# Optimization experiments

Measured on AMD Instinct MI355X. Metric: run time of the kernel, lower is better.

## Reference

```python
import jax, jax.numpy as jnp
import numpy as np

N_H = 896
N_EMB = 300
V_IN = 30000
V_OUT = 30000
B = 64
T_ENC = 40
T_DEC = 40


def gru_cell(x, h, Wih, Whh, bih, bhh):
    # PyTorch GRU cell math
    gi = x @ Wih.T + bih          # [B, 3H]
    gh = h @ Whh.T + bhh          # [B, 3H]
    ir, iz, inn = jnp.split(gi, 3, axis=-1)
    hr, hz, hn = jnp.split(gh, 3, axis=-1)
    r = jax.nn.sigmoid(ir + hr)
    z = jax.nn.sigmoid(iz + hz)
    n = jnp.tanh(inn + r * hn)
    return (1.0 - z) * n + z * h


def run_gru(xs, h0, Wih, Whh, bih, bhh, reverse=False):
    # xs: [T, B, E] -> outputs [T, B, H], final hidden [B, H]
    def step(h, x):
        h2 = gru_cell(x, h, Wih, Whh, bih, bhh)
        return h2, h2
    hT, ys = jax.lax.scan(step, h0, xs, reverse=reverse)
    return ys, hT


def setup_inputs() -> dict:
    key = jax.random.key(0)
    ks = jax.random.split(key, 20)
    s = 0.05
    inp = {
        'x_encoder': jax.random.randint(ks[0], (B, T_ENC), 0, V_IN - 1),
        'x_decoder': jax.random.randint(ks[1], (B, T_DEC), 0, V_OUT - 1),
        'emb_enc': jax.random.normal(ks[2], (V_IN, N_EMB), jnp.float32) * s,
        'Wih_f': jax.random.normal(ks[3], (3 * N_H, N_EMB), jnp.float32) * s,
        'Whh_f': jax.random.normal(ks[4], (3 * N_H, N_H), jnp.float32) * s,
        'bih_f': jnp.zeros((3 * N_H,), jnp.float32),
        'bhh_f': jnp.zeros((3 * N_H,), jnp.float32),
        'Wih_b': jax.random.normal(ks[5], (3 * N_H, N_EMB), jnp.float32) * s,
        'Whh_b': jax.random.normal(ks[6], (3 * N_H, N_H), jnp.float32) * s,
        'bih_b': jnp.zeros((3 * N_H,), jnp.float32),
        'bhh_b': jnp.zeros((3 * N_H,), jnp.float32),
        'emb_dec': jax.random.normal(ks[7], (V_OUT, N_EMB), jnp.float32) * s,
        'Wih_d': jax.random.normal(ks[8], (3 * N_H, N_EMB), jnp.float32) * s,
        'Whh_d': jax.random.normal(ks[9], (3 * N_H, N_H), jnp.float32) * s,
        'bih_d': jnp.zeros((3 * N_H,), jnp.float32),
        'bhh_d': jnp.zeros((3 * N_H,), jnp.float32),
        'fc_W': jax.random.normal(ks[10], (V_OUT, 2 * N_H), jnp.float32) * s,
        'fc_b': jnp.zeros((V_OUT,), jnp.float32),
    }
    return inp


def reference(x_encoder, x_decoder, emb_enc, Wih_f, Whh_f, bih_f, bhh_f,
              Wih_b, Whh_b, bih_b, bhh_b, emb_dec, Wih_d, Whh_d, bih_d,
              bhh_d, fc_W, fc_b):
    Bsz = x_encoder.shape[0]
    h0 = jnp.zeros((Bsz, N_H), jnp.float32)

    # ---- Encoder: bidirectional 1-layer GRU (no padding, full lengths) ----
    xs = emb_enc[x_encoder].transpose(1, 0, 2)          # [Te, B, E]
    y_f, h_f = run_gru(xs, h0, Wih_f, Whh_f, bih_f, bhh_f)
    y_b, h_b = run_gru(xs, h0, Wih_b, Whh_b, bih_b, bhh_b, reverse=True)
    y_enc = (y_f + y_b).transpose(1, 0, 2)              # [B, Te, H] (dirs summed)
    h = h_f + h_b                                       # [B, H]

    # ---- Decoder: per-step GRU + dot-product attention over encoder ----
    xd = emb_dec[x_decoder].transpose(1, 0, 2)          # [Td, B, E]

    def dec_step(h, x):
        h2 = gru_cell(x, h, Wih_d, Whh_d, bih_d, bhh_d)        # [B, H]
        scores = jnp.einsum('bth,bh->bt', y_enc, h2)           # ed_mat
        attn = jax.nn.softmax(scores, axis=1)                  # over Te
        ctx = jnp.einsum('bt,bth->bh', attn, y_enc)            # [B, H]
        logits = jnp.concatenate([h2, ctx], axis=-1) @ fc_W.T + fc_b
        return h2, jax.nn.softmax(logits, axis=-1)

    _, ys = jax.lax.scan(dec_step, h, xd)               # [Td, B, V]
    return ys.transpose(1, 0, 2)                        # [B, Td, V]
```

## Files before the change

### kernel.cpp

```cpp
#include <hip/hip_runtime.h>

#define BB 64
#define TE 40
#define TD 40
#define ED 300
#define EP 320
#define HD 896
#define G3 2688
#define VO 30000
#define VP2 30208
#define KZ 1792
#define KT 28
#define MR 2560
#define NBLK 120

#define FOFF 0
#define BOFF 56
#define DOFF 112
#define AOFF 168
#define TOFF 232
#define FSTR 32

typedef __attribute__((ext_vector_type(8))) __bf16 bf16x8;
typedef __attribute__((ext_vector_type(4))) float f32x4;
typedef __attribute__((ext_vector_type(4))) unsigned int u32x4;
typedef __attribute__((ext_vector_type(4))) unsigned short u16x4;

typedef __attribute__((address_space(1))) const void av1c;
typedef __attribute__((address_space(3))) void av3;

__device__ __forceinline__ float sig_(float x)  { return 1.0f / (1.0f + __expf(-x)); }
__device__ __forceinline__ float tanh_(float x) { return 1.0f - 2.0f / (__expf(2.0f * x) + 1.0f); }

__device__ __forceinline__ void gload_lds16(const __bf16* g, __bf16* l) {
    __builtin_amdgcn_global_load_lds((av1c*)g, (av3*)l, 16, 0, 0);
}

__device__ __forceinline__ bf16x8 ld128_sc(const __bf16* p) {
    bf16x8 r;
    asm volatile("global_load_dwordx4 %0, %1, off sc0 sc1" : "=v"(r) : "v"(p));
    return r;
}
__device__ __forceinline__ f32x4 ldf4_sc(const float* p) {
    f32x4 r;
    asm volatile("global_load_dwordx4 %0, %1, off sc0 sc1" : "=v"(r) : "v"(p));
    return r;
}
__device__ __forceinline__ float ldf_sc(const float* p) {
    float r;
    asm volatile("global_load_dword %0, %1, off sc0 sc1" : "=v"(r) : "v"(p));
    return r;
}
__device__ __forceinline__ void vm_wait0() {
    asm volatile("s_waitcnt vmcnt(0)" ::: "memory");
}
__device__ __forceinline__ void stf_sc(float* p, float v) {
    asm volatile("global_store_dword %0, %1, off sc0 sc1" :: "v"(p), "v"(v) : "memory");
}
__device__ __forceinline__ void sth_sc(__bf16* p, float v) {
    unsigned int u = (unsigned int)__builtin_bit_cast(unsigned short, (__bf16)v);
    asm volatile("global_store_short %0, %1, off sc0 sc1" :: "v"(p), "v"(u) : "memory");
}
__device__ __forceinline__ void sti_sc(int* p, int v) {
    asm volatile("global_store_dword %0, %1, off sc0 sc1" :: "v"(p), "v"(v) : "memory");
}
__device__ __forceinline__ void spin_ge(const int* p, int target) {
    int v;
    for (;;) {
        asm volatile("global_load_dword %0, %1, off sc0 sc1\n\ts_waitcnt vmcnt(0)"
                     : "=v"(v) : "v"(p) : "memory");
        if (v >= target) break;
        __builtin_amdgcn_s_sleep(1);
    }
}

__device__ __forceinline__ size_t hblk(int b, int c) {
    return ((size_t)(c >> 4) * 64 + b) * 16 + (c & 15);
}

__device__ __forceinline__ void stage_w(__bf16* wlds, const float* __restrict__ W, int c0)
{
    const int tid = threadIdx.x;
    for (int ch = tid; ch < 48 * 224; ch += 256) {
        const int lr = ch / 224, c4 = (ch % 224) * 4;
        const int g = lr >> 4, rr = lr & 15;
        const int kk = c4 >> 5, hi = (c4 & 31) >> 3, j = c4 & 7;
        const float4 v = *(const float4*)&W[(size_t)(g * HD + c0 + rr) * HD + c4];
        __bf16* d = &wlds[((g * 28 + kk) * 64 + hi * 16 + rr) * 8 + j];
        d[0] = (__bf16)v.x; d[1] = (__bf16)v.y; d[2] = (__bf16)v.z; d[3] = (__bf16)v.w;
    }
}

struct GiReg { float g0[4], g1[4], g2[4]; };

__device__ __forceinline__ GiReg gi_prefetch(const float* __restrict__ GIt,
                                             int c, int w, int hi)
{
    GiReg r;
#pragma unroll
    for (int rg = 0; rg < 4; ++rg) {
        const float* gp = GIt + (size_t)(16 * w + hi * 4 + rg) * G3 + c;
        r.g0[rg] = gp[0]; r.g1[rg] = gp[HD]; r.g2[rg] = gp[2 * HD];
    }
    return r;
}

__device__ __forceinline__ void gru_step(
    const __bf16* __restrict__ hcurB, const float* __restrict__ hcurF,
    const __bf16* __restrict__ wlds, const GiReg& gi,
    float bh0, float bh1, float bh2,
    float* __restrict__ hnF, __bf16* __restrict__ hnB,
    float* __restrict__ yencD,
    int tt,
    __bf16* __restrict__ zrow,
    int c0, int lane, int w)
{
    const int r16 = lane & 15, hi = lane >> 4;
    const int c = c0 + r16;
    const int colblk = c0 >> 4;
    const int brow = 16 * w;

    bf16x8 afr[28];
    const __bf16* ap = hcurB + ((size_t)(hi >> 1) * 64 + brow + r16) * 16 + (hi & 1) * 8;
#pragma unroll
    for (int kk = 0; kk < 28; ++kk) afr[kk] = ld128_sc(ap + kk * 2048);
    float hp[4];
#pragma unroll
    for (int rg = 0; rg < 4; ++rg)
        hp[rg] = ldf_sc(hcurF + ((size_t)colblk * 64 + brow + hi * 4 + rg) * 16 + r16);
    vm_wait0();
    __builtin_amdgcn_sched_barrier(0);

    f32x4 a0 = {0.f, 0.f, 0.f, 0.f}, a1 = a0, a2 = a0;
#pragma unroll
    for (int kk = 0; kk < 28; ++kk) {
        const bf16x8 b0 = *(const bf16x8*)&wlds[(kk) * 512 + lane * 8];
        const bf16x8 b1 = *(const bf16x8*)&wlds[(28 + kk) * 512 + lane * 8];
        const bf16x8 b2 = *(const bf16x8*)&wlds[(56 + kk) * 512 + lane * 8];
        a0 = __builtin_amdgcn_mfma_f32_16x16x32_bf16(afr[kk], b0, a0, 0, 0, 0);
        a1 = __builtin_amdgcn_mfma_f32_16x16x32_bf16(afr[kk], b1, a1, 0, 0, 0);
        a2 = __builtin_amdgcn_mfma_f32_16x16x32_bf16(afr[kk], b2, a2, 0, 0, 0);
    }

#pragma unroll
    for (int rg = 0; rg < 4; ++rg) {
        const int b = brow + hi * 4 + rg;
        const float rr = sig_(gi.g0[rg] + a0[rg] + bh0);
        const float zz = sig_(gi.g1[rg] + a1[rg] + bh1);
        const float nn = tanh_(gi.g2[rg] + rr * (a2[rg] + bh2));
        const float hnew = (1.0f - zz) * nn + zz * hp[rg];
        const size_t so = ((size_t)colblk * 64 + b) * 16 + r16;
        stf_sc(hnF + so, hnew);
        sth_sc(hnB + so, hnew);
        if (yencD) stf_sc(yencD + (((size_t)colblk * 64 + b) * TE + tt) * 16 + r16, hnew);
        if (zrow)  zrow[(size_t)b * KZ + c] = (__bf16)hnew;
    }
}

__device__ __forceinline__ void attn_step(
    const float* __restrict__ yencL, float* __restrict__ h2s,
    float* __restrict__ scL, float* __restrict__ attwL,
    const float* __restrict__ h2g, int b, __bf16* __restrict__ zr,
    int* __restrict__ myflag, int postval)
{
    const int tid = threadIdx.x, lane = tid & 63, w = tid >> 6;

    const float a0 = ldf_sc(h2g + hblk(b, tid));
    const float a1 = ldf_sc(h2g + hblk(b, tid + 256));
    const float a2 = ldf_sc(h2g + hblk(b, tid + 512));
    const float a3 = (tid < HD - 768) ? ldf_sc(h2g + hblk(b, tid + 768)) : 0.0f;
    vm_wait0();
    __builtin_amdgcn_sched_barrier(0);
    h2s[tid] = a0; h2s[tid + 256] = a1; h2s[tid + 512] = a2;
    if (tid < HD - 768) h2s[tid + 768] = a3;
    __syncthreads();
    if (tid == 0) sti_sc(myflag, postval);

    const float2* h22 = (const float2*)h2s;
    for (int t = w; t < TE; t += 4) {
        const float2* y2 = (const float2*)(yencL + t * HD);
        float p = 0.f;
#pragma unroll
        for (int it = 0; it < HD / 128; ++it) {
            const float2 ya = y2[lane + it * 64];
            const float2 hb2 = h22[lane + it * 64];
            p += ya.x * hb2.x + ya.y * hb2.y;
        }
        p += __shfl_down(p, 32); p += __shfl_down(p, 16); p += __shfl_down(p, 8);
        p += __shfl_down(p, 4);  p += __shfl_down(p, 2);  p += __shfl_down(p, 1);
        if (lane == 0) scL[t] = p;
    }
    __syncthreads();

    float m = scL[0];
    for (int t = 1; t < TE; ++t) m = fmaxf(m, scL[t]);
    float s = 0.f;
    for (int t = 0; t < TE; ++t) s += __expf(scL[t] - m);
    const float inv = 1.0f / s;
    if (tid < TE) attwL[tid] = __expf(scL[tid] - m) * inv;
    __syncthreads();

    for (int c = tid; c < HD; c += 256) {
        float acc = 0.f;
#pragma unroll
        for (int t = 0; t < TE; ++t) acc += attwL[t] * yencL[t * HD + c];
        zr[(size_t)b * KZ + HD + c] = (__bf16)acc;
    }
    __syncthreads();
}

__global__ __launch_bounds__(256, 1) void recur(
    const float* __restrict__ GIf, const float* __restrict__ GIb,
    const float* __restrict__ GId,
    const float* __restrict__ WhhF, const float* __restrict__ WhhB,
    const float* __restrict__ WhhD,
    const float* __restrict__ bhhF, const float* __restrict__ bhhB,
    const float* __restrict__ bhhD,
    float* __restrict__ heF, __bf16* __restrict__ heB,
    float* __restrict__ hdF, __bf16* __restrict__ hdB,
    float* __restrict__ yenc_f, float* __restrict__ yenc_b,
    __bf16* __restrict__ Zb, int* __restrict__ flags)
{
    __shared__ __align__(16) char smem[147456];
    __bf16* wlds  = (__bf16*)smem;
    float*  yencL = (float*)smem;
    float*  h2s   = (float*)(smem + 143360);
    float*  scL   = (float*)(smem + 146944);
    float*  attwL = (float*)(smem + 147136);

    const int gid = blockIdx.x;
    const int tid = threadIdx.x;
    const int lane = tid & 63, w = tid >> 6;
    const int r16 = lane & 15, hi = lane >> 4;
    const size_t S = (size_t)BB * HD;

    float bb0 = 0.f, bb1 = 0.f, bb2 = 0.f;
    GiReg gi;

    if (gid < 112) {
        const int dir = (gid >= 56) ? 1 : 0;
        const int gloc = dir ? gid - 56 : gid;
        const int c0e = gloc * 16;
        const float* GIe  = dir ? GIb : GIf;
        const float* bhhE = dir ? bhhB : bhhF;
        float* yencD = dir ? yenc_b : yenc_f;
        const int foff = dir ? BOFF : FOFF;

        stage_w(wlds, dir ? WhhB : WhhF, c0e);
        const int ce = c0e + r16;
        bb0 = bhhE[ce]; bb1 = bhhE[HD + ce]; bb2 = bhhE[2 * HD + ce];
        gi = gi_prefetch(GIe + (size_t)(dir ? TE - 1 : 0) * BB * G3, ce, w, hi);
        __syncthreads();

        for (int t = 0; t < TE; ++t) {
            if (t > 0) {
                if (tid < 56) spin_ge(flags + (foff + tid) * FSTR, t);
                __syncthreads();
            }
            GiReg gin = gi;
            if (t + 1 < TE) {
                const int ttn = dir ? (TE - 2 - t) : (t + 1);
                gin = gi_prefetch(GIe + (size_t)ttn * BB * G3, ce, w, hi);
            }
            const int tt = dir ? (TE - 1 - t) : t;
            gru_step(heB + (size_t)(dir * 2 + (t & 1)) * S,
                     heF + (size_t)(dir * 2 + (t & 1)) * S,
                     wlds, gi, bb0, bb1, bb2,
                     heF + (size_t)(dir * 2 + ((t + 1) & 1)) * S,
                     heB + (size_t)(dir * 2 + ((t + 1) & 1)) * S,
                     yencD, tt, nullptr, c0e, lane, w);
            vm_wait0();
            __syncthreads();
            if (tid == 0) sti_sc(flags + (foff + gloc) * FSTR, t + 1);
            gi = gin;
        }
    }

    if (tid < 112) spin_ge(flags + tid * FSTR, TE);
    __syncthreads();

    {
        const int i0 = gid * 256 + tid;
        const int i1 = i0 + NBLK * 256;
        const bool has1 = (i1 < BB * HD);
        const float f0 = ldf_sc(&heF[0 * S + i0]);
        const float b0 = ldf_sc(&heF[2 * S + i0]);
        const float f1 = has1 ? ldf_sc(&heF[0 * S + i1]) : 0.f;
        const float b1 = has1 ? ldf_sc(&heF[2 * S + i1]) : 0.f;
        vm_wait0();
        __builtin_amdgcn_sched_barrier(0);
        const float v0 = f0 + b0;
        stf_sc(&hdF[i0], v0); sth_sc(&hdB[i0], v0);
        if (has1) { const float v1 = f1 + b1; stf_sc(&hdF[i1], v1); sth_sc(&hdB[i1], v1); }
    }
    if (gid < 56) {
        stage_w(wlds, WhhD, gid * 16);
        const int cd = gid * 16 + r16;
        bb0 = bhhD[cd]; bb1 = bhhD[HD + cd]; bb2 = bhhD[2 * HD + cd];
        gi = gi_prefetch(GId, cd, w, hi);
    }
    vm_wait0();
    __syncthreads();
    if (tid == 0) sti_sc(flags + (TOFF + gid) * FSTR, 1);
    if (tid < 120) spin_ge(flags + (TOFF + tid) * FSTR, 1);
    __syncthreads();

    if (gid < 56) {
        for (int p = 0; p < TD; ++p) {
            if (p > 0 && tid < 56) spin_ge(flags + (DOFF + tid) * FSTR, p);
            if (p >= 4 && tid >= 64 && tid < 128)
                spin_ge(flags + (AOFF + tid - 64) * FSTR, p - 3);
            __syncthreads();
            GiReg gin = gi;
            if (p + 1 < TD)
                gin = gi_prefetch(GId + (size_t)(p + 1) * BB * G3, gid * 16 + r16, w, hi);
            gru_step(hdB + (size_t)(p & 3) * S, hdF + (size_t)(p & 3) * S,
                     wlds, gi, bb0, bb1, bb2,
                     hdF + (size_t)((p + 1) & 3) * S, hdB + (size_t)((p + 1) & 3) * S,
                     nullptr, 0, Zb + (size_t)p * BB * KZ, gid * 16, lane, w);
            vm_wait0();
            __syncthreads();
            if (tid == 0) sti_sc(flags + (DOFF + gid) * FSTR, p + 1);
            gi = gin;
        }
    } else {
        const int b = gid - 56;
        const float* sf = yenc_f;
        const float* sb = yenc_b;
        for (int it = 0; it < 7; ++it) {
            const int i = it * 1280 + tid;
            f32x4 a_[5], b_[5];
            int g_[5], t_[5], c_[5];
#pragma unroll
            for (int u = 0; u < 5; ++u) {
                const int j = i + u * 256;
                g_[u] = j / 160;
                const int rem = j - g_[u] * 160;
                t_[u] = rem >> 2;
                c_[u] = (rem & 3) * 4;
                const size_t sa = (((size_t)g_[u] * 64 + b) * TE + t_[u]) * 16 + c_[u];
                a_[u] = ldf4_sc(sf + sa);
                b_[u] = ldf4_sc(sb + sa);
            }
            vm_wait0();
            __builtin_amdgcn_sched_barrier(0);
#pragma unroll
            for (int u = 0; u < 5; ++u)
                *(f32x4*)&yencL[(size_t)t_[u] * HD + g_[u] * 16 + c_[u]] = a_[u] + b_[u];
        }
        __syncthreads();
        for (int s = 0; s < TD; ++s) {
            if (tid < 56) spin_ge(flags + (DOFF + tid) * FSTR, s + 1);
            __syncthreads();
            attn_step(yencL, h2s, scL, attwL, hdF + (size_t)((s + 1) & 3) * S,
                      b, Zb + (size_t)s * BB * KZ, flags + (AOFF + b) * FSTR, s + 1);
        }
    }
}

__global__ __launch_bounds__(256) void gemm_bt(
    const __bf16* __restrict__ A0, const __bf16* __restrict__ B0,
    float* __restrict__ C0, const float* __restrict__ bias0,
    const __bf16* __restrict__ A1, const __bf16* __restrict__ B1,
    float* __restrict__ C1, const float* __restrict__ bias1,
    int M, int N, int K)
{
    constexpr int BM = 128, BN = 128, BK = 32;
    constexpr int FM = 4, FN = 4;

    const __bf16* A = A0; const __bf16* Bp = B0;
    float* C = C0; const float* bias = bias0;
    if (blockIdx.z == 1) { A = A1; Bp = B1; C = C1; bias = bias1; }

    __shared__ __bf16 Ash[2][BM * BK];
    __shared__ __bf16 Bsh[2][BN * BK];

    const int tid  = threadIdx.x;
    const int lane = tid & 63;
    const int wave = tid >> 6;
    const int wr = wave >> 1, wc = wave & 1;

    const int nwg = gridDim.x * gridDim.y;
    const int orig = blockIdx.y * gridDim.x + blockIdx.x;
    const int q = nwg >> 3, r = nwg & 7;
    const int xcd = orig & 7, idx = orig >> 3;
    const int wg = (xcd < r ? xcd * (q + 1) : r * (q + 1) + (xcd - r) * q) + idx;
    const int mtiles = gridDim.y;
    const long tileM = (long)(wg % mtiles) * BM;
    const long tileN = (long)(wg / mtiles) * BN;

    const int r16 = lane & 15;
    const int hi  = lane >> 4;

    f32x4 acc[FM][FN];
    const f32x4 zero = {0.f, 0.f, 0.f, 0.f};
#pragma unroll
    for (int m = 0; m < FM; ++m)
#pragma unroll
        for (int n = 0; n < FN; ++n) acc[m][n] = zero;

    const int srow = wave * 32 + (lane >> 2);
    const int schunk = (lane & 3) * 8;
    const __bf16* gA = A + (size_t)(tileM + srow) * K + schunk;
    const __bf16* gB = Bp + (size_t)(tileN + srow) * K + schunk;
    const size_t kstep16 = (size_t)16 * K;
    const int lofs = (wave * 32) * BK;

#define STAGE_T(k0_, sel_)                                            \
    do {                                                              \
        gload_lds16(gA + (k0_), &Ash[sel_][lofs]);                    \
        gload_lds16(gA + (k0_) + kstep16, &Ash[sel_][lofs + 16 * BK]);\
        gload_lds16(gB + (k0_), &Bsh[sel_][lofs]);                    \
        gload_lds16(gB + (k0_) + kstep16, &Bsh[sel_][lofs + 16 * BK]);\
    } while (0)

    STAGE_T(0, 0);
    int cur = 0;
    for (int k0 = BK; k0 < K; k0 += BK) {
        STAGE_T(k0, cur ^ 1);
        asm volatile("s_waitcnt vmcnt(4)" ::: "memory");
        __builtin_amdgcn_s_barrier();
        __builtin_amdgcn_sched_barrier(0);

        bf16x8 af[FM], bfr[FN];
#pragma unroll
        for (int m = 0; m < FM; ++m)
            af[m] = *(const bf16x8*)&Ash[cur][(wr * 64 + m * 16 + r16) * BK + hi * 8];
#pragma unroll
        for (int n = 0; n < FN; ++n)
            bfr[n] = *(const bf16x8*)&Bsh[cur][(wc * 64 + n * 16 + r16) * BK + hi * 8];
#pragma unroll
        for (int m = 0; m < FM; ++m)
#pragma unroll
            for (int n = 0; n < FN; ++n)
                acc[m][n] = __builtin_amdgcn_mfma_f32_16x16x32_bf16(af[m], bfr[n], acc[m][n], 0, 0, 0);

        __builtin_amdgcn_sched_barrier(0);
        __builtin_amdgcn_s_barrier();
        __builtin_amdgcn_sched_barrier(0);
        cur ^= 1;
    }
    asm volatile("s_waitcnt vmcnt(0)" ::: "memory");
    __builtin_amdgcn_s_barrier();
    __builtin_amdgcn_sched_barrier(0);
    {
        bf16x8 af[FM], bfr[FN];
#pragma unroll
        for (int m = 0; m < FM; ++m)
            af[m] = *(const bf16x8*)&Ash[cur][(wr * 64 + m * 16 + r16) * BK + hi * 8];
#pragma unroll
        for (int n = 0; n < FN; ++n)
            bfr[n] = *(const bf16x8*)&Bsh[cur][(wc * 64 + n * 16 + r16) * BK + hi * 8];
#pragma unroll
        for (int m = 0; m < FM; ++m)
#pragma unroll
            for (int n = 0; n < FN; ++n)
                acc[m][n] = __builtin_amdgcn_mfma_f32_16x16x32_bf16(af[m], bfr[n], acc[m][n], 0, 0, 0);
    }
#undef STAGE_T

#pragma unroll
    for (int m = 0; m < FM; ++m) {
#pragma unroll
        for (int n = 0; n < FN; ++n) {
            const long gcol = tileN + wc * 64 + n * 16 + r16;
            const float bv = bias ? bias[gcol] : 0.0f;
#pragma unroll
            for (int rr = 0; rr < 4; ++rr) {
                const long grow = tileM + wr * 64 + m * 16 + hi * 4 + rr;
                C[grow * N + gcol] = acc[m][n][rr] + bv;
            }
        }
    }
}

__global__ __launch_bounds__(512, 2) void gemm_fc(
    const __bf16* __restrict__ A,
    const __bf16* __restrict__ B,
    float* __restrict__ C,
    const float* __restrict__ bias)
{
    __shared__ __bf16 lds[65536];

    const int tid = threadIdx.x;
    const int lane = tid & 63;
    const int wave = tid >> 6;
    const int wm = wave >> 2;
    const int wn = wave & 3;
    const int r16 = lane & 15, hi = lane >> 4;

    const int nwg = gridDim.x * gridDim.y;
    const int orig = blockIdx.y * gridDim.x + blockIdx.x;
    const int q_ = nwg >> 3, r_ = nwg & 7;
    const int xcd = orig & 7, idx = orig >> 3;
    const int wg = (xcd < r_ ? xcd * (q_ + 1) : r_ * (q_ + 1) + (xcd - r_) * q_) + idx;
    const int mtiles = gridDim.y;
    const long tileM = (long)(wg % mtiles) * 256;
    const long tileN = (long)(wg / mtiles) * 256;

    const int srow0 = wave * 8 + (lane >> 3);
    const int scol  = ((lane & 7) ^ (lane >> 3)) * 8;
    const __bf16* gAh[2] = { A + (size_t)tileM * KZ, A + (size_t)(tileM + 128) * KZ };
    const __bf16* gBh[2] = { B + (size_t)tileN * KZ, B + (size_t)(tileN + 128) * KZ };
    auto Abase = [](int buf, int h) { return (buf * 2 + h) * 8192; };
    auto Bbase = [](int buf, int h) { return 32768 + (buf * 2 + h) * 8192; };
    auto stage = [&](const __bf16* gph, int kt, int lbase) {
        const __bf16* g0 = gph + (size_t)srow0 * KZ + kt * 64 + scol;
        gload_lds16(g0, &lds[lbase + wave * 512]);
        gload_lds16(g0 + (size_t)64 * KZ, &lds[lbase + (8 + wave) * 512]);
    };
    const int cbx0 = (((0 * 64) + hi * 16) ^ ((r16 & 7) << 4)) >> 1;
    const int cbx1 = (((1 * 64) + hi * 16) ^ ((r16 & 7) << 4)) >> 1;

    f32x4 acc[8][4];
    const f32x4 zero = {0.f, 0.f, 0.f, 0.f};
#pragma unroll
    for (int m = 0; m < 8; ++m)
#pragma unroll
        for (int n = 0; n < 4; ++n) acc[m][n] = zero;

    stage(gAh[0], 0, Abase(0, 0));
    stage(gAh[1], 0, Abase(0, 1));
    stage(gBh[0], 0, Bbase(0, 0));
    stage(gBh[1], 0, Bbase(0, 1));
    stage(gBh[0], 1, Bbase(1, 0));
    stage(gBh[1], 1, Bbase(1, 1));
    asm volatile("s_waitcnt vmcnt(4)" ::: "memory");
    __builtin_amdgcn_s_barrier();

    for (int kt = 0; kt < KT; ++kt) {
        const int buf = kt & 1;
        const int kn1 = (kt + 1 < KT) ? kt + 1 : 0;
        const int kn2 = (kt + 2 < KT) ? kt + 2 : 0;
        const int Ab = Abase(buf, wm);
        const int Bb = Bbase(buf, wn >> 1);
        bf16x8 bfr[4][2];
#pragma unroll
        for (int q = 0; q < 4; ++q) {
            if (q == 0) {
#pragma unroll
                for (int n = 0; n < 4; ++n) {
                    const int rowB = (wn & 1) * 64 + n * 16 + r16;
                    bfr[n][0] = *(const bf16x8*)&lds[Bb + rowB * 64 + cbx0];
                    bfr[n][1] = *(const bf16x8*)&lds[Bb + rowB * 64 + cbx1];
                }
            }
            bf16x8 af[2][2];
#pragma unroll
            for (int mm = 0; mm < 2; ++mm) {
                const int rowA = (q * 2 + mm) * 16 + r16;
                af[mm][0] = *(const bf16x8*)&lds[Ab + rowA * 64 + cbx0];
                af[mm][1] = *(const bf16x8*)&lds[Ab + rowA * 64 + cbx1];
            }
            if (q == 0)      stage(gAh[0], kn1, Abase(buf ^ 1, 0));
            else if (q == 1) stage(gAh[1], kn1, Abase(buf ^ 1, 1));
            else if (q == 2) stage(gBh[0], kn2, Bbase(buf, 0));
            else {
                stage(gBh[1], kn2, Bbase(buf, 1));
                asm volatile("s_waitcnt vmcnt(4)" ::: "memory");
            }
            __builtin_amdgcn_s_barrier();
            asm volatile("s_waitcnt lgkmcnt(0)" ::: "memory");
            __builtin_amdgcn_sched_barrier(0);
            __builtin_amdgcn_s_setprio(1);
#pragma unroll
            for (int mm = 0; mm < 2; ++mm)
#pragma unroll
                for (int n = 0; n < 4; ++n) {
                    acc[q * 2 + mm][n] = __builtin_amdgcn_mfma_f32_16x16x32_bf16(
                        af[mm][0], bfr[n][0], acc[q * 2 + mm][n], 0, 0, 0);
                    acc[q * 2 + mm][n] = __builtin_amdgcn_mfma_f32_16x16x32_bf16(
                        af[mm][1], bfr[n][1], acc[q * 2 + mm][n], 0, 0, 0);
                }
            __builtin_amdgcn_s_setprio(0);
            __builtin_amdgcn_sched_barrier(0);
            __builtin_amdgcn_s_barrier();
        }
    }
    asm volatile("s_waitcnt vmcnt(0)" ::: "memory");

#pragma unroll
    for (int m = 0; m < 8; ++m) {
#pragma unroll
        for (int n = 0; n < 4; ++n) {
            const long gcol = tileN + wn * 64 + n * 16 + r16;
            if (gcol >= VO) continue;
            const float bv = bias[gcol];
#pragma unroll
            for (int rr = 0; rr < 4; ++rr) {
                const long grow = tileM + wm * 128 + m * 16 + hi * 4 + rr;
                const long t = grow >> 6, b = grow & 63;
                C[(b * TD + t) * VO + gcol] = acc[m][n][rr] + bv;
            }
        }
    }
}

__global__ __launch_bounds__(256) void conv_pad(const float* __restrict__ src,
                                                __bf16* __restrict__ dst,
                                                int Rout, int Rin, int Kout, int Kin)
{
    size_t i = (size_t)blockIdx.x * 256 + threadIdx.x;
    const size_t total = (size_t)Rout * Kout;
    const size_t stride = (size_t)gridDim.x * 256;
    for (; i < total; i += stride) {
        int k = (int)(i % Kout);
        int r = (int)(i / Kout);
        float v = (r < Rin && k < Kin) ? src[(size_t)r * Kin + k] : 0.0f;
        dst[i] = (__bf16)v;
    }
}

__global__ __launch_bounds__(256) void conv_fcw(const float* __restrict__ src,
                                                __bf16* __restrict__ dst)
{
    const size_t total4 = (size_t)VP2 * KZ / 4;
    for (size_t i = (size_t)blockIdx.x * 256 + threadIdx.x; i < total4;
         i += (size_t)gridDim.x * 256) {
        const size_t e0 = i * 4;
        const int r = (int)(e0 / KZ);
        u16x4 o;
        if (r < VO) {
            const float4 x = *(const float4*)&src[e0];
            o.x = __builtin_bit_cast(unsigned short, (__bf16)x.x);
            o.y = __builtin_bit_cast(unsigned short, (__bf16)x.y);
            o.z = __builtin_bit_cast(unsigned short, (__bf16)x.z);
            o.w = __builtin_bit_cast(unsigned short, (__bf16)x.w);
        } else {
            o.x = 0; o.y = 0; o.z = 0; o.w = 0;
        }
        *(u16x4*)&dst[e0] = o;
    }
}

__global__ __launch_bounds__(256) void gather_embed(const int* __restrict__ tok,
                                                    const float* __restrict__ emb,
                                                    __bf16* __restrict__ X)
{
    int i = blockIdx.x * 256 + threadIdx.x;
    const int total = TE * BB * EP;
    for (; i < total; i += gridDim.x * 256) {
        int e = i % EP;
        int row = i / EP;
        int t = row >> 6, b = row & 63;
        float v = 0.0f;
        if (e < ED) v = emb[(size_t)tok[b * TE + t] * ED + e];
        X[i] = (__bf16)v;
    }
}

__global__ __launch_bounds__(1024) void softmax_kernel(float* __restrict__ out)
{
    __shared__ float row[VO];
    __shared__ float red[16];
    __shared__ float red2[16];
    const size_t base = (size_t)blockIdx.x * VO;
    const int tid = threadIdx.x;
    const int lane = tid & 63, w = tid >> 6;

    float m = -1e30f;
    for (int ch = tid; ch < VO / 4; ch += 1024) {
        const float4 x = *(const float4*)&out[base + ch * 4];
        *(float4*)&row[ch * 4] = x;
        m = fmaxf(fmaxf(fmaxf(m, x.x), x.y), fmaxf(x.z, x.w));
    }
    m = fmaxf(m, __shfl_down(m, 32)); m = fmaxf(m, __shfl_down(m, 16));
    m = fmaxf(m, __shfl_down(m, 8));  m = fmaxf(m, __shfl_down(m, 4));
    m = fmaxf(m, __shfl_down(m, 2));  m = fmaxf(m, __shfl_down(m, 1));
    if (lane == 0) red[w] = m;
    __syncthreads();
    if (tid == 0) {
        float mm = red[0];
#pragma unroll
        for (int i = 1; i < 16; ++i) mm = fmaxf(mm, red[i]);
        red[0] = mm;
    }
    __syncthreads();
    m = red[0];

    float s = 0.0f;
    for (int v = tid; v < VO; v += 1024) {
        const float e = __expf(row[v] - m);
        row[v] = e;
        s += e;
    }
    s += __shfl_down(s, 32); s += __shfl_down(s, 16); s += __shfl_down(s, 8);
    s += __shfl_down(s, 4);  s += __shfl_down(s, 2);  s += __shfl_down(s, 1);
    if (lane == 0) red2[w] = s;
    __syncthreads();
    if (tid == 0) {
        float ss = red2[0];
#pragma unroll
        for (int i = 1; i < 16; ++i) ss += red2[i];
        red2[0] = ss;
    }
    __syncthreads();
    s = red2[0];

    const float inv = 1.0f / s;
    for (int ch = tid; ch < VO / 4; ch += 1024) {
        float4 x = *(const float4*)&row[ch * 4];
        x.x *= inv; x.y *= inv; x.z *= inv; x.w *= inv;
        *(float4*)&out[base + ch * 4] = x;
    }
}

extern "C" void kernel_launch(void* const* d_in, const int* in_sizes, int n_in,
                              void* d_out, int out_size, void* d_ws, size_t ws_size,
                              hipStream_t stream)
{
    if (n_in < 18) return;
    const int*   x_enc   = (const int*)d_in[0];
    const int*   x_dec   = (const int*)d_in[1];
    const float* emb_enc = (const float*)d_in[2];
    const float* Wih_f   = (const float*)d_in[3];
    const float* Whh_f   = (const float*)d_in[4];
    const float* bih_f   = (const float*)d_in[5];
    const float* bhh_f   = (const float*)d_in[6];
    const float* Wih_b   = (const float*)d_in[7];
    const float* Whh_b   = (const float*)d_in[8];
    const float* bih_b   = (const float*)d_in[9];
    const float* bhh_b   = (const float*)d_in[10];
    const float* emb_dec = (const float*)d_in[11];
    const float* Wih_d   = (const float*)d_in[12];
    const float* Whh_d   = (const float*)d_in[13];
    const float* bih_d   = (const float*)d_in[14];
    const float* bhh_d   = (const float*)d_in[15];
    const float* fc_W    = (const float*)d_in[16];
    const float* fc_b    = (const float*)d_in[17];
    float* out = (float*)d_out;

    size_t off = 0;
    auto alloc = [&](size_t bytes) -> void* {
        void* p = (char*)d_ws + off;
        off = (off + bytes + 255) & ~(size_t)255;
        return p;
    };
    __bf16* fcWb   = (__bf16*)alloc((size_t)VP2 * KZ * 2);
    __bf16* WihFb  = (__bf16*)alloc((size_t)G3 * EP * 2);
    __bf16* WihBb  = (__bf16*)alloc((size_t)G3 * EP * 2);
    __bf16* WihDb  = (__bf16*)alloc((size_t)G3 * EP * 2);
    __bf16* Xe     = (__bf16*)alloc((size_t)MR * EP * 2);
    __bf16* Xd     = (__bf16*)alloc((size_t)MR * EP * 2);
    float*  GIf    = (float*)alloc((size_t)MR * G3 * 4);
    float*  GIb    = (float*)alloc((size_t)MR * G3 * 4);
    float*  GId    = (float*)alloc((size_t)MR * G3 * 4);
    __bf16* Zb     = (__bf16*)alloc((size_t)MR * KZ * 2);
    float*  yenc_f = (float*)alloc((size_t)BB * TE * HD * 4);
    float*  yenc_b = (float*)alloc((size_t)BB * TE * HD * 4);
    float*  hdF    = (float*)alloc((size_t)4 * BB * HD * 4);
    __bf16* hdB    = (__bf16*)alloc((size_t)4 * BB * HD * 2);
    char* zero_start = (char*)d_ws + off;
    float*  heF    = (float*)alloc((size_t)4 * BB * HD * 4);
    __bf16* heB    = (__bf16*)alloc((size_t)4 * BB * HD * 2);
    int*    flags  = (int*)alloc(512 * FSTR * 4);
    size_t zero_bytes = (size_t)(((char*)d_ws + off) - zero_start);
    if (off > ws_size) return;

    hipMemsetAsync(zero_start, 0, zero_bytes, stream);
    conv_fcw<<<8192, 256, 0, stream>>>(fc_W, fcWb);
    conv_pad<<<3360, 256, 0, stream>>>(Wih_f, WihFb, G3, G3, EP, ED);
    conv_pad<<<3360, 256, 0, stream>>>(Wih_b, WihBb, G3, G3, EP, ED);
    conv_pad<<<3360, 256, 0, stream>>>(Wih_d, WihDb, G3, G3, EP, ED);
    gather_embed<<<3200, 256, 0, stream>>>(x_enc, emb_enc, Xe);
    gather_embed<<<3200, 256, 0, stream>>>(x_dec, emb_dec, Xd);

    gemm_bt<<<dim3(G3 / 128, MR / 128, 2), 256, 0, stream>>>(
        Xe, WihFb, GIf, bih_f, Xe, WihBb, GIb, bih_b, MR, G3, EP);
    gemm_bt<<<dim3(G3 / 128, MR / 128, 1), 256, 0, stream>>>(
        Xd, WihDb, GId, bih_d, nullptr, nullptr, nullptr, nullptr, MR, G3, EP);

    recur<<<NBLK, 256, 0, stream>>>(GIf, GIb, GId, Whh_f, Whh_b, Whh_d,
                                    bhh_f, bhh_b, bhh_d,
                                    heF, heB, hdF, hdB, yenc_f, yenc_b, Zb, flags);

    gemm_fc<<<dim3(VP2 / 256, MR / 256), 512, 0, stream>>>(Zb, fcWb, out, fc_b);

    softmax_kernel<<<BB * TD, 1024, 0, stream>>>(out);
}
```

Baseline: 1.019 ms.

## Fuse FC GEMM into persistent recurrence kernel with flag-gated tile queue

Folds the output projection GEMM into the persistent recurrence kernel. It launches 248 blocks of 512 threads. The 128 extra blocks pull FC tiles from an atomic work queue and start a tile as soon as the decoder steps it needs have produced their hidden states and context rows, signalled through new per-batch flags. This overlaps the large vocab GEMM with the serial decoder recurrence instead of running it afterwards. In exchange it widens the recurrence blocks to 512 threads with half of them idle during GRU steps, adds spin-waiting and atomics, and adds a bounded spin that could quietly proceed on a timeout.

```diff
diff --git a/kernel.cpp b/kernel.cpp
--- a/kernel.cpp
+++ b/kernel.cpp
@@ -13,12 +13,17 @@
 #define KT 28
 #define MR 2560
 #define NBLK 120
+#define NWB 248
+#define NTN 118
+#define NTILE (NTN * 10)
 
 #define FOFF 0
 #define BOFF 56
 #define DOFF 112
 #define AOFF 168
 #define TOFF 232
+#define ZOFF 352
+#define QOFF 448
 #define FSTR 32
 
 typedef __attribute__((ext_vector_type(8))) __bf16 bf16x8;
@@ -34,6 +39,9 @@
 
 __device__ __forceinline__ void gload_lds16(const __bf16* g, __bf16* l) {
     __builtin_amdgcn_global_load_lds((av1c*)g, (av3*)l, 16, 0, 0);
+}
+__device__ __forceinline__ void gload_lds16_sc(const __bf16* g, __bf16* l) {
+    __builtin_amdgcn_global_load_lds((av1c*)g, (av3*)l, 16, 0, 17);
 }
 
 __device__ __forceinline__ bf16x8 ld128_sc(const __bf16* p) {
@@ -71,6 +79,15 @@
                      : "=v"(v) : "v"(p) : "memory");
         if (v >= target) break;
         __builtin_amdgcn_s_sleep(1);
+    }
+}
+__device__ __forceinline__ void spinb(const int* p, int target) {
+    for (int it = 0; it < (1 << 20); ++it) {
+        int v;
+        asm volatile("global_load_dword %0, %1, off sc0 sc1\n\ts_waitcnt vmcnt(0)"
+                     : "=v"(v) : "v"(p) : "memory");
+        if (v >= target) return;
+        __builtin_amdgcn_s_sleep(16);
     }
 }
 
@@ -110,8 +127,7 @@
     const __bf16* __restrict__ wlds, const GiReg& gi,
     float bh0, float bh1, float bh2,
     float* __restrict__ hnF, __bf16* __restrict__ hnB,
-    float* __restrict__ yencD,
-    int tt,
+    float* __restrict__ yencD, int tt,
     __bf16* __restrict__ zrow,
     int c0, int lane, int w)
 {
@@ -153,31 +169,30 @@
         stf_sc(hnF + so, hnew);
         sth_sc(hnB + so, hnew);
         if (yencD) stf_sc(yencD + (((size_t)colblk * 64 + b) * TE + tt) * 16 + r16, hnew);
-        if (zrow)  zrow[(size_t)b * KZ + c] = (__bf16)hnew;
-    }
-}
-
-__device__ __forceinline__ void attn_step(
+        if (zrow)  sth_sc(zrow + (size_t)b * KZ + c, hnew);
+    }
+}
+
+__device__ __forceinline__ void attn_step512(
     const float* __restrict__ yencL, float* __restrict__ h2s,
     float* __restrict__ scL, float* __restrict__ attwL,
     const float* __restrict__ h2g, int b, __bf16* __restrict__ zr,
-    int* __restrict__ myflag, int postval)
+    int* __restrict__ myflag, int* __restrict__ zflag, int postval)
 {
     const int tid = threadIdx.x, lane = tid & 63, w = tid >> 6;
 
-    const float a0 = ldf_sc(h2g + hblk(b, tid));
-    const float a1 = ldf_sc(h2g + hblk(b, tid + 256));
-    const float a2 = ldf_sc(h2g + hblk(b, tid + 512));
-    const float a3 = (tid < HD - 768) ? ldf_sc(h2g + hblk(b, tid + 768)) : 0.0f;
+    float a0 = 0.f, a1 = 0.f;
+    if (tid < HD) a0 = ldf_sc(h2g + hblk(b, tid));
+    if (tid + 512 < HD) a1 = ldf_sc(h2g + hblk(b, tid + 512));
     vm_wait0();
     __builtin_amdgcn_sched_barrier(0);
-    h2s[tid] = a0; h2s[tid + 256] = a1; h2s[tid + 512] = a2;
-    if (tid < HD - 768) h2s[tid + 768] = a3;
+    if (tid < HD) h2s[tid] = a0;
+    if (tid + 512 < HD) h2s[tid + 512] = a1;
     __syncthreads();
     if (tid == 0) sti_sc(myflag, postval);
 
     const float2* h22 = (const float2*)h2s;
-    for (int t = w; t < TE; t += 4) {
+    for (int t = w; t < TE; t += 8) {
         const float2* y2 = (const float2*)(yencL + t * HD);
         float p = 0.f;
 #pragma unroll
@@ -200,16 +215,18 @@
     if (tid < TE) attwL[tid] = __expf(scL[tid] - m) * inv;
     __syncthreads();
 
-    for (int c = tid; c < HD; c += 256) {
+    for (int c = tid; c < HD; c += 512) {
         float acc = 0.f;
 #pragma unroll
         for (int t = 0; t < TE; ++t) acc += attwL[t] * yencL[t * HD + c];
-        zr[(size_t)b * KZ + HD + c] = (__bf16)acc;
-    }
+        sth_sc(zr + (size_t)b * KZ + HD + c, acc);
+    }
+    vm_wait0();
     __syncthreads();
-}
-
-__global__ __launch_bounds__(256, 1) void recur(
+    if (tid == 0) sti_sc(zflag, postval);
+}
+
+__global__ __launch_bounds__(512, 1) void recur(
     const float* __restrict__ GIf, const float* __restrict__ GIb,
     const float* __restrict__ GId,
     const float* __restrict__ WhhF, const float* __restrict__ WhhB,
@@ -219,7 +236,9 @@
     float* __restrict__ heF, __bf16* __restrict__ heB,
     float* __restrict__ hdF, __bf16* __restrict__ hdB,
     float* __restrict__ yenc_f, float* __restrict__ yenc_b,
-    __bf16* __restrict__ Zb, int* __restrict__ flags)
+    __bf16* __restrict__ Zb, int* __restrict__ flags,
+    const __bf16* __restrict__ fcW, float* __restrict__ outC,
+    const float* __restrict__ fcb)
 {
     __shared__ __align__(16) char smem[147456];
     __bf16* wlds  = (__bf16*)smem;
@@ -227,6 +246,7 @@
     float*  h2s   = (float*)(smem + 143360);
     float*  scL   = (float*)(smem + 146944);
     float*  attwL = (float*)(smem + 147136);
+    volatile int* shtile = (volatile int*)(smem + 147400);
 
     const int gid = blockIdx.x;
     const int tid = threadIdx.x;
@@ -234,126 +254,263 @@
     const int r16 = lane & 15, hi = lane >> 4;
     const size_t S = (size_t)BB * HD;
 
-    float bb0 = 0.f, bb1 = 0.f, bb2 = 0.f;
-    GiReg gi;
-
-    if (gid < 112) {
-        const int dir = (gid >= 56) ? 1 : 0;
-        const int gloc = dir ? gid - 56 : gid;
-        const int c0e = gloc * 16;
-        const float* GIe  = dir ? GIb : GIf;
-        const float* bhhE = dir ? bhhB : bhhF;
-        float* yencD = dir ? yenc_b : yenc_f;
-        const int foff = dir ? BOFF : FOFF;
-
-        stage_w(wlds, dir ? WhhB : WhhF, c0e);
-        const int ce = c0e + r16;
-        bb0 = bhhE[ce]; bb1 = bhhE[HD + ce]; bb2 = bhhE[2 * HD + ce];
-        gi = gi_prefetch(GIe + (size_t)(dir ? TE - 1 : 0) * BB * G3, ce, w, hi);
+    if (gid < NBLK) {
+        float bb0 = 0.f, bb1 = 0.f, bb2 = 0.f;
+        GiReg gi;
+
+        if (gid < 112) {
+            const int dir = (gid >= 56) ? 1 : 0;
+            const int gloc = dir ? gid - 56 : gid;
+            const int c0e = gloc * 16;
+            const float* GIe  = dir ? GIb : GIf;
+            const float* bhhE = dir ? bhhB : bhhF;
+            float* yencD = dir ? yenc_b : yenc_f;
+            const int foff = dir ? BOFF : FOFF;
+            const int ce = c0e + r16;
+
+            stage_w(wlds, dir ? WhhB : WhhF, c0e);
+            if (tid < 256) {
+                bb0 = bhhE[ce]; bb1 = bhhE[HD + ce]; bb2 = bhhE[2 * HD + ce];
+                gi = gi_prefetch(GIe + (size_t)(dir ? TE - 1 : 0) * BB * G3, ce, w, hi);
+            }
+            __syncthreads();
+
+            for (int t = 0; t < TE; ++t) {
+                if (t > 0) {
+                    if (tid < 56) spin_ge(flags + (foff + tid) * FSTR, t);
+                    __syncthreads();
+                }
+                const int tt = dir ? (TE - 1 - t) : t;
+                if (tid < 256)
+                    gru_step(heB + (size_t)(dir * 2 + (t & 1)) * S,
+                             heF + (size_t)(dir * 2 + (t & 1)) * S,
+                             wlds, gi, bb0, bb1, bb2,
+                             heF + (size_t)(dir * 2 + ((t + 1) & 1)) * S,
+                             heB + (size_t)(dir * 2 + ((t + 1) & 1)) * S,
+                             yencD, tt, nullptr, c0e, lane, w);
+                vm_wait0();
+                __syncthreads();
+                if (tid == 0) sti_sc(flags + (foff + gloc) * FSTR, t + 1);
+                if (t + 1 < TE && tid < 256) {
+                    const int ttn = dir ? (TE - 2 - t) : (t + 1);
+                    gi = gi_prefetch(GIe + (size_t)ttn * BB * G3, ce, w, hi);
+                }
+            }
+        }
+
+        if (tid < 112) spin_ge(flags + tid * FSTR, TE);
         __syncthreads();
 
-        for (int t = 0; t < TE; ++t) {
-            if (t > 0) {
-                if (tid < 56) spin_ge(flags + (foff + tid) * FSTR, t);
-                __syncthreads();
-            }
-            GiReg gin = gi;
-            if (t + 1 < TE) {
-                const int ttn = dir ? (TE - 2 - t) : (t + 1);
-                gin = gi_prefetch(GIe + (size_t)ttn * BB * G3, ce, w, hi);
-            }
-            const int tt = dir ? (TE - 1 - t) : t;
-            gru_step(heB + (size_t)(dir * 2 + (t & 1)) * S,
-                     heF + (size_t)(dir * 2 + (t & 1)) * S,
-                     wlds, gi, bb0, bb1, bb2,
-                     heF + (size_t)(dir * 2 + ((t + 1) & 1)) * S,
-                     heB + (size_t)(dir * 2 + ((t + 1) & 1)) * S,
-                     yencD, tt, nullptr, c0e, lane, w);
-            vm_wait0();
-            __syncthreads();
-            if (tid == 0) sti_sc(flags + (foff + gloc) * FSTR, t + 1);
-            gi = gin;
-        }
-    }
-
-    if (tid < 112) spin_ge(flags + tid * FSTR, TE);
-    __syncthreads();
-
-    {
-        const int i0 = gid * 256 + tid;
-        const int i1 = i0 + NBLK * 256;
-        const bool has1 = (i1 < BB * HD);
-        const float f0 = ldf_sc(&heF[0 * S + i0]);
-        const float b0 = ldf_sc(&heF[2 * S + i0]);
-        const float f1 = has1 ? ldf_sc(&heF[0 * S + i1]) : 0.f;
-        const float b1 = has1 ? ldf_sc(&heF[2 * S + i1]) : 0.f;
-        vm_wait0();
-        __builtin_amdgcn_sched_barrier(0);
-        const float v0 = f0 + b0;
-        stf_sc(&hdF[i0], v0); sth_sc(&hdB[i0], v0);
-        if (has1) { const float v1 = f1 + b1; stf_sc(&hdF[i1], v1); sth_sc(&hdB[i1], v1); }
-    }
-    if (gid < 56) {
-        stage_w(wlds, WhhD, gid * 16);
-        const int cd = gid * 16 + r16;
-        bb0 = bhhD[cd]; bb1 = bhhD[HD + cd]; bb2 = bhhD[2 * HD + cd];
-        gi = gi_prefetch(GId, cd, w, hi);
-    }
-    vm_wait0();
-    __syncthreads();
-    if (tid == 0) sti_sc(flags + (TOFF + gid) * FSTR, 1);
-    if (tid < 120) spin_ge(flags + (TOFF + tid) * FSTR, 1);
-    __syncthreads();
-
-    if (gid < 56) {
-        for (int p = 0; p < TD; ++p) {
-            if (p > 0 && tid < 56) spin_ge(flags + (DOFF + tid) * FSTR, p);
-            if (p >= 4 && tid >= 64 && tid < 128)
-                spin_ge(flags + (AOFF + tid - 64) * FSTR, p - 3);
-            __syncthreads();
-            GiReg gin = gi;
-            if (p + 1 < TD)
-                gin = gi_prefetch(GId + (size_t)(p + 1) * BB * G3, gid * 16 + r16, w, hi);
-            gru_step(hdB + (size_t)(p & 3) * S, hdF + (size_t)(p & 3) * S,
-                     wlds, gi, bb0, bb1, bb2,
-                     hdF + (size_t)((p + 1) & 3) * S, hdB + (size_t)((p + 1) & 3) * S,
-                     nullptr, 0, Zb + (size_t)p * BB * KZ, gid * 16, lane, w);
-            vm_wait0();
-            __syncthreads();
-            if (tid == 0) sti_sc(flags + (DOFF + gid) * FSTR, p + 1);
-            gi = gin;
-        }
-    } else {
-        const int b = gid - 56;
-        const float* sf = yenc_f;
-        const float* sb = yenc_b;
-        for (int it = 0; it < 7; ++it) {
-            const int i = it * 1280 + tid;
-            f32x4 a_[5], b_[5];
-            int g_[5], t_[5], c_[5];
-#pragma unroll
-            for (int u = 0; u < 5; ++u) {
-                const int j = i + u * 256;
-                g_[u] = j / 160;
-                const int rem = j - g_[u] * 160;
-                t_[u] = rem >> 2;
-                c_[u] = (rem & 3) * 4;
-                const size_t sa = (((size_t)g_[u] * 64 + b) * TE + t_[u]) * 16 + c_[u];
-                a_[u] = ldf4_sc(sf + sa);
-                b_[u] = ldf4_sc(sb + sa);
-            }
+        {
+            const int i0 = gid * 256 + tid;
+            const int i1 = i0 + NBLK * 256;
+            const bool has0 = (i0 < BB * HD);
+            const bool has1 = (i1 < BB * HD);
+            const float f0 = has0 ? ldf_sc(&heF[0 * S + i0]) : 0.f;
+            const float b0 = has0 ? ldf_sc(&heF[2 * S + i0]) : 0.f;
+            const float f1 = has1 ? ldf_sc(&heF[0 * S + i1]) : 0.f;
+            const float b1 = has1 ? ldf_sc(&heF[2 * S + i1]) : 0.f;
             vm_wait0();
             __builtin_amdgcn_sched_barrier(0);
-#pragma unroll
-            for (int u = 0; u < 5; ++u)
-                *(f32x4*)&yencL[(size_t)t_[u] * HD + g_[u] * 16 + c_[u]] = a_[u] + b_[u];
+            if (has0) { const float v0 = f0 + b0; stf_sc(&hdF[i0], v0); sth_sc(&hdB[i0], v0); }
+            if (has1) { const float v1 = f1 + b1; stf_sc(&hdF[i1], v1); sth_sc(&hdB[i1], v1); }
         }
+        if (gid < 56) {
+            stage_w(wlds, WhhD, gid * 16);
+            if (tid < 256) {
+                const int cd = gid * 16 + r16;
+                bb0 = bhhD[cd]; bb1 = bhhD[HD + cd]; bb2 = bhhD[2 * HD + cd];
+                gi = gi_prefetch(GId, cd, w, hi);
+            }
+        }
+        vm_wait0();
         __syncthreads();
-        for (int s = 0; s < TD; ++s) {
-            if (tid < 56) spin_ge(flags + (DOFF + tid) * FSTR, s + 1);
+        if (tid == 0) sti_sc(flags + (TOFF + gid) * FSTR, 1);
+        if (tid < 120) spin_ge(flags + (TOFF + tid) * FSTR, 1);
+        __syncthreads();
+
+        if (gid < 56) {
+            for (int p = 0; p < TD; ++p) {
+                if (p > 0 && tid < 56) spin_ge(flags + (DOFF + tid) * FSTR, p);
+                if (p >= 4 && tid >= 64 && tid < 128)
+                    spin_ge(flags + (AOFF + tid - 64) * FSTR, p - 3);
+                __syncthreads();
+                if (tid < 256)
+                    gru_step(hdB + (size_t)(p & 3) * S, hdF + (size_t)(p & 3) * S,
+                             wlds, gi, bb0, bb1, bb2,
+                             hdF + (size_t)((p + 1) & 3) * S, hdB + (size_t)((p + 1) & 3) * S,
+                             nullptr, 0, Zb + (size_t)p * BB * KZ, gid * 16, lane, w);
+                vm_wait0();
+                __syncthreads();
+                if (tid == 0) sti_sc(flags + (DOFF + gid) * FSTR, p + 1);
+                if (p + 1 < TD && tid < 256)
+                    gi = gi_prefetch(GId + (size_t)(p + 1) * BB * G3, gid * 16 + r16, w, hi);
+            }
+        } else {
+            const int b = gid - 56;
+            const float* sf = yenc_f;
+            const float* sb = yenc_b;
+            for (int it = 0; it < 4; ++it) {
+                f32x4 a_[5], b_[5];
+                int tt_[5], gg_[5], cc_[5]; bool ok[5];
+#pragma unroll
+                for (int u = 0; u < 5; ++u) {
+                    const int j = it * 2560 + u * 512 + tid;
+                    ok[u] = (j < 8960);
+                    if (ok[u]) {
+                        gg_[u] = j / 160;
+                        const int rem = j - gg_[u] * 160;
+                        tt_[u] = rem >> 2;
+                        cc_[u] = (rem & 3) * 4;
+                        const size_t sa = (((size_t)gg_[u] * 64 + b) * TE + tt_[u]) * 16 + cc_[u];
+                        a_[u] = ldf4_sc(sf + sa);
+                        b_[u] = ldf4_sc(sb + sa);
+                    }
+                }
+                vm_wait0();
+                __builtin_amdgcn_sched_barrier(0);
+#pragma unroll
+                for (int u = 0; u < 5; ++u)
+                    if (ok[u])
+                        *(f32x4*)&yencL[(size_t)tt_[u] * HD + gg_[u] * 16 + cc_[u]] = a_[u] + b_[u];
+            }
             __syncthreads();
-            attn_step(yencL, h2s, scL, attwL, hdF + (size_t)((s + 1) & 3) * S,
-                      b, Zb + (size_t)s * BB * KZ, flags + (AOFF + b) * FSTR, s + 1);
+            for (int s = 0; s < TD; ++s) {
+                if (tid < 56) spin_ge(flags + (DOFF + tid) * FSTR, s + 1);
+                __syncthreads();
+                attn_step512(yencL, h2s, scL, attwL, hdF + (size_t)((s + 1) & 3) * S,
+                             b, Zb + (size_t)s * BB * KZ,
+                             flags + (AOFF + b) * FSTR, flags + (ZOFF + b) * FSTR, s + 1);
+            }
+        }
+    }
+
+    {
+        __bf16* lds = (__bf16*)smem;
+        const int wave = tid >> 6;
+        const int wm = wave >> 2, wn = wave & 3;
+        int* qcnt = flags + QOFF * FSTR;
+
+        const int srow0 = wave * 8 + (lane >> 3);
+        const int scol  = ((lane & 7) ^ (lane >> 3)) * 8;
+        const int cbx0 = ((hi * 16) ^ ((r16 & 7) << 4)) >> 1;
+        const int cbx1 = ((64 + hi * 16) ^ ((r16 & 7) << 4)) >> 1;
+
+        for (;;) {
+            if (tid == 0) {
+                const int tl = __hip_atomic_fetch_add(qcnt, 1, __ATOMIC_RELAXED,
+                                                      __HIP_MEMORY_SCOPE_AGENT);
+                *shtile = tl;
+            }
+            __syncthreads();
+            const int tile = *shtile;
+            if (tile >= NTILE) break;
+            const int mt = tile / NTN, nt = tile - mt * NTN;
+            const int need = 4 * mt + 4;
+            if (tid < 56) spinb(flags + (DOFF + tid) * FSTR, need);
+            if (tid >= 64 && tid < 128) spinb(flags + (ZOFF + tid - 64) * FSTR, need);
+            __syncthreads();
+
+            const long tileM = (long)mt * 256;
+            const long tileN = (long)nt * 256;
+            const __bf16* gAh[2] = { Zb + (size_t)tileM * KZ, Zb + (size_t)(tileM + 128) * KZ };
+            const __bf16* gBh[2] = { fcW + (size_t)tileN * KZ, fcW + (size_t)(tileN + 128) * KZ };
+            auto Abase = [](int buf, int h) { return (buf * 2 + h) * 8192; };
+            auto Bbase = [](int buf, int h) { return 32768 + (buf * 2 + h) * 8192; };
+            auto stageA = [&](const __bf16* gph, int kt, int lbase) {
+                const __bf16* g0 = gph + (size_t)srow0 * KZ + kt * 64 + scol;
+                gload_lds16_sc(g0, &lds[lbase + wave * 512]);
+                gload_lds16_sc(g0 + (size_t)64 * KZ, &lds[lbase + (8 + wave) * 512]);
+            };
+            auto stageB = [&](const __bf16* gph, int kt, int lbase) {
+                const __bf16* g0 = gph + (size_t)srow0 * KZ + kt * 64 + scol;
+                gload_lds16(g0, &lds[lbase + wave * 512]);
+                gload_lds16(g0 + (size_t)64 * KZ, &lds[lbase + (8 + wave) * 512]);
+            };
+
+            f32x4 acc[8][4];
+            const f32x4 zero = {0.f, 0.f, 0.f, 0.f};
+#pragma unroll
+            for (int m = 0; m < 8; ++m)
+#pragma unroll
+                for (int n = 0; n < 4; ++n) acc[m][n] = zero;
+
+            stageA(gAh[0], 0, Abase(0, 0));
+            stageA(gAh[1], 0, Abase(0, 1));
+            stageB(gBh[0], 0, Bbase(0, 0));
+            stageB(gBh[1], 0, Bbase(0, 1));
+            stageB(gBh[0], 1, Bbase(1, 0));
+            stageB(gBh[1], 1, Bbase(1, 1));
+            asm volatile("s_waitcnt vmcnt(4)" ::: "memory");
+            __builtin_amdgcn_s_barrier();
+
+            for (int kt = 0; kt < KT; ++kt) {
+                const int buf = kt & 1;
+                const int kn1 = (kt + 1 < KT) ? kt + 1 : 0;
+                const int kn2 = (kt + 2 < KT) ? kt + 2 : 0;
+                const int Ab = Abase(buf, wm);
+                const int Bb = Bbase(buf, wn >> 1);
+                bf16x8 bfr[4][2];
+#pragma unroll
+                for (int q = 0; q < 4; ++q) {
+                    if (q == 0) {
+#pragma unroll
+                        for (int n = 0; n < 4; ++n) {
+                            const int rowB = (wn & 1) * 64 + n * 16 + r16;
+                            bfr[n][0] = *(const bf16x8*)&lds[Bb + rowB * 64 + cbx0];
+                            bfr[n][1] = *(const bf16x8*)&lds[Bb + rowB * 64 + cbx1];
+                        }
+                    }
+                    bf16x8 af[2][2];
+#pragma unroll
+                    for (int mm = 0; mm < 2; ++mm) {
+                        const int rowA = (q * 2 + mm) * 16 + r16;
+                        af[mm][0] = *(const bf16x8*)&lds[Ab + rowA * 64 + cbx0];
+                        af[mm][1] = *(const bf16x8*)&lds[Ab + rowA * 64 + cbx1];
+                    }
+                    if (q == 0)      stageA(gAh[0], kn1, Abase(buf ^ 1, 0));
+                    else if (q == 1) stageA(gAh[1], kn1, Abase(buf ^ 1, 1));
+                    else if (q == 2) stageB(gBh[0], kn2, Bbase(buf, 0));
+                    else {
+                        stageB(gBh[1], kn2, Bbase(buf, 1));
+                        asm volatile("s_waitcnt vmcnt(4)" ::: "memory");
+                    }
+                    __builtin_amdgcn_s_barrier();
+                    asm volatile("s_waitcnt lgkmcnt(0)" ::: "memory");
+                    __builtin_amdgcn_sched_barrier(0);
+                    __builtin_amdgcn_s_setprio(1);
+#pragma unroll
+                    for (int mm = 0; mm < 2; ++mm)
+#pragma unroll
+                        for (int n = 0; n < 4; ++n) {
+                            acc[q * 2 + mm][n] = __builtin_amdgcn_mfma_f32_16x16x32_bf16(
+                                af[mm][0], bfr[n][0], acc[q * 2 + mm][n], 0, 0, 0);
+                            acc[q * 2 + mm][n] = __builtin_amdgcn_mfma_f32_16x16x32_bf16(
+                                af[mm][1], bfr[n][1], acc[q * 2 + mm][n], 0, 0, 0);
+                        }
+                    __builtin_amdgcn_s_setprio(0);
+                    __builtin_amdgcn_sched_barrier(0);
+                    __builtin_amdgcn_s_barrier();
+                }
+            }
+            asm volatile("s_waitcnt vmcnt(0)" ::: "memory");
+
+#pragma unroll
+            for (int m = 0; m < 8; ++m) {
+#pragma unroll
+                for (int n = 0; n < 4; ++n) {
+                    const long gcol = tileN + wn * 64 + n * 16 + r16;
+                    if (gcol >= VO) continue;
+                    const float bv = fcb[gcol];
+#pragma unroll
+                    for (int rr = 0; rr < 4; ++rr) {
+                        const long grow = tileM + wm * 128 + m * 16 + hi * 4 + rr;
+                        const long t = grow >> 6, b = grow & 63;
+                        outC[(b * TD + t) * VO + gcol] = acc[m][n][rr] + bv;
+                    }
+                }
+            }
+            __syncthreads();
         }
     }
 }
@@ -469,128 +626,6 @@
             for (int rr = 0; rr < 4; ++rr) {
                 const long grow = tileM + wr * 64 + m * 16 + hi * 4 + rr;
                 C[grow * N + gcol] = acc[m][n][rr] + bv;
-            }
-        }
-    }
-}
-
-__global__ __launch_bounds__(512, 2) void gemm_fc(
-    const __bf16* __restrict__ A,
-    const __bf16* __restrict__ B,
-    float* __restrict__ C,
-    const float* __restrict__ bias)
-{
-    __shared__ __bf16 lds[65536];
-
-    const int tid = threadIdx.x;
-    const int lane = tid & 63;
-    const int wave = tid >> 6;
-    const int wm = wave >> 2;
-    const int wn = wave & 3;
-    const int r16 = lane & 15, hi = lane >> 4;
-
-    const int nwg = gridDim.x * gridDim.y;
-    const int orig = blockIdx.y * gridDim.x + blockIdx.x;
-    const int q_ = nwg >> 3, r_ = nwg & 7;
-    const int xcd = orig & 7, idx = orig >> 3;
-    const int wg = (xcd < r_ ? xcd * (q_ + 1) : r_ * (q_ + 1) + (xcd - r_) * q_) + idx;
-    const int mtiles = gridDim.y;
-    const long tileM = (long)(wg % mtiles) * 256;
-    const long tileN = (long)(wg / mtiles) * 256;
-
-    const int srow0 = wave * 8 + (lane >> 3);
-    const int scol  = ((lane & 7) ^ (lane >> 3)) * 8;
-    const __bf16* gAh[2] = { A + (size_t)tileM * KZ, A + (size_t)(tileM + 128) * KZ };
-    const __bf16* gBh[2] = { B + (size_t)tileN * KZ, B + (size_t)(tileN + 128) * KZ };
-    auto Abase = [](int buf, int h) { return (buf * 2 + h) * 8192; };
-    auto Bbase = [](int buf, int h) { return 32768 + (buf * 2 + h) * 8192; };
-    auto stage = [&](const __bf16* gph, int kt, int lbase) {
-        const __bf16* g0 = gph + (size_t)srow0 * KZ + kt * 64 + scol;
-        gload_lds16(g0, &lds[lbase + wave * 512]);
-        gload_lds16(g0 + (size_t)64 * KZ, &lds[lbase + (8 + wave) * 512]);
-    };
-    const int cbx0 = (((0 * 64) + hi * 16) ^ ((r16 & 7) << 4)) >> 1;
-    const int cbx1 = (((1 * 64) + hi * 16) ^ ((r16 & 7) << 4)) >> 1;
-
-    f32x4 acc[8][4];
-    const f32x4 zero = {0.f, 0.f, 0.f, 0.f};
-#pragma unroll
-    for (int m = 0; m < 8; ++m)
-#pragma unroll
-        for (int n = 0; n < 4; ++n) acc[m][n] = zero;
-
-    stage(gAh[0], 0, Abase(0, 0));
-    stage(gAh[1], 0, Abase(0, 1));
-    stage(gBh[0], 0, Bbase(0, 0));
-    stage(gBh[1], 0, Bbase(0, 1));
-    stage(gBh[0], 1, Bbase(1, 0));
-    stage(gBh[1], 1, Bbase(1, 1));
-    asm volatile("s_waitcnt vmcnt(4)" ::: "memory");
-    __builtin_amdgcn_s_barrier();
-
-    for (int kt = 0; kt < KT; ++kt) {
-        const int buf = kt & 1;
-        const int kn1 = (kt + 1 < KT) ? kt + 1 : 0;
-        const int kn2 = (kt + 2 < KT) ? kt + 2 : 0;
-        const int Ab = Abase(buf, wm);
-        const int Bb = Bbase(buf, wn >> 1);
-        bf16x8 bfr[4][2];
-#pragma unroll
-        for (int q = 0; q < 4; ++q) {
-            if (q == 0) {
-#pragma unroll
-                for (int n = 0; n < 4; ++n) {
-                    const int rowB = (wn & 1) * 64 + n * 16 + r16;
-                    bfr[n][0] = *(const bf16x8*)&lds[Bb + rowB * 64 + cbx0];
-                    bfr[n][1] = *(const bf16x8*)&lds[Bb + rowB * 64 + cbx1];
-                }
-            }
-            bf16x8 af[2][2];
-#pragma unroll
-            for (int mm = 0; mm < 2; ++mm) {
-                const int rowA = (q * 2 + mm) * 16 + r16;
-                af[mm][0] = *(const bf16x8*)&lds[Ab + rowA * 64 + cbx0];
-                af[mm][1] = *(const bf16x8*)&lds[Ab + rowA * 64 + cbx1];
-            }
-            if (q == 0)      stage(gAh[0], kn1, Abase(buf ^ 1, 0));
-            else if (q == 1) stage(gAh[1], kn1, Abase(buf ^ 1, 1));
-            else if (q == 2) stage(gBh[0], kn2, Bbase(buf, 0));
-            else {
-                stage(gBh[1], kn2, Bbase(buf, 1));
-                asm volatile("s_waitcnt vmcnt(4)" ::: "memory");
-            }
-            __builtin_amdgcn_s_barrier();
-            asm volatile("s_waitcnt lgkmcnt(0)" ::: "memory");
-            __builtin_amdgcn_sched_barrier(0);
-            __builtin_amdgcn_s_setprio(1);
-#pragma unroll
-            for (int mm = 0; mm < 2; ++mm)
-#pragma unroll
-                for (int n = 0; n < 4; ++n) {
-                    acc[q * 2 + mm][n] = __builtin_amdgcn_mfma_f32_16x16x32_bf16(
-                        af[mm][0], bfr[n][0], acc[q * 2 + mm][n], 0, 0, 0);
-                    acc[q * 2 + mm][n] = __builtin_amdgcn_mfma_f32_16x16x32_bf16(
-                        af[mm][1], bfr[n][1], acc[q * 2 + mm][n], 0, 0, 0);
-                }
-            __builtin_amdgcn_s_setprio(0);
-            __builtin_amdgcn_sched_barrier(0);
-            __builtin_amdgcn_s_barrier();
-        }
-    }
-    asm volatile("s_waitcnt vmcnt(0)" ::: "memory");
-
-#pragma unroll
-    for (int m = 0; m < 8; ++m) {
-#pragma unroll
-        for (int n = 0; n < 4; ++n) {
-            const long gcol = tileN + wn * 64 + n * 16 + r16;
-            if (gcol >= VO) continue;
-            const float bv = bias[gcol];
-#pragma unroll
-            for (int rr = 0; rr < 4; ++rr) {
-                const long grow = tileM + wm * 128 + m * 16 + hi * 4 + rr;
-                const long t = grow >> 6, b = grow & 63;
-                C[(b * TD + t) * VO + gcol] = acc[m][n][rr] + bv;
             }
         }
     }
@@ -770,11 +805,10 @@
     gemm_bt<<<dim3(G3 / 128, MR / 128, 1), 256, 0, stream>>>(
         Xd, WihDb, GId, bih_d, nullptr, nullptr, nullptr, nullptr, MR, G3, EP);
 
-    recur<<<NBLK, 256, 0, stream>>>(GIf, GIb, GId, Whh_f, Whh_b, Whh_d,
-                                    bhh_f, bhh_b, bhh_d,
-                                    heF, heB, hdF, hdB, yenc_f, yenc_b, Zb, flags);
-
-    gemm_fc<<<dim3(VP2 / 256, MR / 256), 512, 0, stream>>>(Zb, fcWb, out, fc_b);
+    recur<<<NWB, 512, 0, stream>>>(GIf, GIb, GId, Whh_f, Whh_b, Whh_d,
+                                   bhh_f, bhh_b, bhh_d,
+                                   heF, heB, hdF, hdB, yenc_f, yenc_b, Zb, flags,
+                                   fcWb, out, fc_b);
 
     softmax_kernel<<<BB * TD, 1024, 0, stream>>>(out);
 }
```

Result: faster. 919.1 us (-9.8%).
